# Optimization experiments

Measured on AMD Instinct MI355X. Metric: run time of the kernel, lower is better.

The kernel has to match this reference:

```python
import jax, jax.numpy as jnp
import numpy as np


def setup_inputs() -> dict:
    key = jax.random.key(0)
    kq, kk, kv, km, kb = jax.random.split(key, 5)
    B, H, S, D = 4, 16, 2048, 64
    Q = jax.random.normal(kq, (B, H, S, D), dtype=jnp.float32)
    K = jax.random.normal(kk, (B, H, S, D), dtype=jnp.float32)
    V = jax.random.normal(kv, (B, H, S, D), dtype=jnp.float32)
    # key-padding style mask, broadcasts over query dim; 0 -> masked
    mask = jax.random.randint(km, (B, 1, 1, S), 0, 2, dtype=jnp.int32)
    attn_bias = jax.random.normal(kb, (1, H, S, S), dtype=jnp.float32)
    return {"Q": Q, "K": K, "V": V, "mask": mask, "attn_bias": attn_bias}


def reference(Q, K, V, mask, attn_bias):
    d_k = Q.shape[-1]
    scale = 1.0 / jnp.sqrt(jnp.asarray(d_k, Q.dtype))
    # [B,H,Sq,Sk] scores
    scores = jnp.einsum("bhqd,bhkd->bhqk", Q, K) * scale
    scores = scores + attn_bias
    scores = jnp.where(mask == 0, jnp.asarray(-1e9, scores.dtype), scores)
    attn = jax.nn.softmax(scores, axis=-1)
    # dropout is identity in eval/reference mode
    output = jnp.einsum("bhqk,bhkd->bhqd", attn, V)
    return output, attn
```

## Files before the change

### kernel.cpp

```cpp
#include <hip/hip_runtime.h>

#define NB 4
#define NH 16
#define NS 2048
#define ND 64

typedef __attribute__((ext_vector_type(8))) short short8;
typedef __attribute__((ext_vector_type(4))) short short4v;
typedef __attribute__((ext_vector_type(4))) float floatx4;
typedef __attribute__((ext_vector_type(2))) float floatx2;

__device__ __forceinline__ unsigned short f2bf(float f) {
  unsigned u = __builtin_bit_cast(unsigned, f);
  u = (u + 0x7FFFu + ((u >> 16) & 1u)) >> 16;
  return (unsigned short)u;
}
__device__ __forceinline__ float bf2f(unsigned short s) {
  unsigned u = ((unsigned)s) << 16;
  return __builtin_bit_cast(float, u);
}

__global__ __launch_bounds__(256) void prep_k_kernel(const float* __restrict__ K,
                                                     unsigned short* __restrict__ kb) {
  size_t i = ((size_t)blockIdx.x * 256 + threadIdx.x) * 4;
  floatx4 v = *(const floatx4*)(K + i);
  unsigned long long o = 0;
  o |= (unsigned long long)f2bf(v[0]);
  o |= (unsigned long long)f2bf(v[1]) << 16;
  o |= (unsigned long long)f2bf(v[2]) << 32;
  o |= (unsigned long long)f2bf(v[3]) << 48;
  *(unsigned long long*)(kb + i) = o;
}

__global__ __launch_bounds__(256) void prep_vt_kernel(const float* __restrict__ V,
                                                      unsigned short* __restrict__ vt) {
  __shared__ float tile[64][65];
  int kc = blockIdx.x & 31;
  int bh = blockIdx.x >> 5;
  int k0 = kc * 64;
  const float* src = V + ((size_t)bh * NS + k0) * ND;
  int t = threadIdx.x;
  int r0 = t >> 4;
  int c = (t & 15) * 4;
  for (int rr = 0; rr < 4; ++rr) {
    int r = rr * 16 + r0;
    floatx4 v = *(const floatx4*)(src + (size_t)r * ND + c);
    tile[r][c + 0] = v[0]; tile[r][c + 1] = v[1];
    tile[r][c + 2] = v[2]; tile[r][c + 3] = v[3];
  }
  __syncthreads();
  unsigned short* dst = vt + (size_t)bh * ND * NS + k0;
  for (int i = 0; i < 16; ++i) {
    int lin = i * 256 + t;
    int d = lin >> 6, k = lin & 63;
    dst[(size_t)d * NS + k] = f2bf(tile[k][d]);
  }
}

__global__ __launch_bounds__(1024) void attn_kernel(
    const float* __restrict__ Q,
    const unsigned short* __restrict__ Kb,
    const unsigned short* __restrict__ VT,
    const int* __restrict__ mask,
    const float* __restrict__ bias,
    float* __restrict__ out,
    float* __restrict__ attn) {
  extern __shared__ char smem[];
  unsigned short* P = (unsigned short*)smem;
  float* sums = (float*)(smem + 32 * 2052 * 2);
  const int PST = 2052;

  const int bid = blockIdx.x;
  const int b = bid & 3;
  const int hq = bid >> 2;
  const int qt = hq & 63;
  const int h = hq >> 6;
  const int q0 = qt * 32;

  const int tid = threadIdx.x;
  const int wave = tid >> 6;
  const int lane = tid & 63;
  const int lg = lane >> 4;
  const int lc = lane & 15;
  const int lg4 = lg * 4;
  const int lg8 = lg * 8;

  const size_t bh = (size_t)(b * NH + h);

  short8 aq[2][2];
#pragma unroll
  for (int qh = 0; qh < 2; ++qh) {
    const float* qrow = Q + (bh * NS + (size_t)(q0 + qh * 16 + lc)) * ND + lg8;
#pragma unroll
    for (int t = 0; t < 2; ++t) {
      floatx4 f0 = *(const floatx4*)(qrow + t * 32);
      floatx4 f1 = *(const floatx4*)(qrow + t * 32 + 4);
      short8 a;
      a[0] = (short)f2bf(f0[0]); a[1] = (short)f2bf(f0[1]);
      a[2] = (short)f2bf(f0[2]); a[3] = (short)f2bf(f0[3]);
      a[4] = (short)f2bf(f1[0]); a[5] = (short)f2bf(f1[1]);
      a[6] = (short)f2bf(f1[2]); a[7] = (short)f2bf(f1[3]);
      aq[qh][t] = a;
    }
  }

  const float* bp[2][4];
#pragma unroll
  for (int qh = 0; qh < 2; ++qh)
#pragma unroll
    for (int r = 0; r < 4; ++r)
      bp[qh][r] = bias + ((size_t)h * NS + (size_t)(q0 + qh * 16 + lg4 + r)) * NS + lc;
  const int* mp = mask + b * NS + lc;
  const unsigned short* kp = Kb + bh * NS * ND + (size_t)lc * ND + lg8;

  float psum[2][4] = {{0.f, 0.f, 0.f, 0.f}, {0.f, 0.f, 0.f, 0.f}};
  const int kb0 = wave * 128;

#pragma unroll 2
  for (int it = 0; it < 8; ++it) {
    const int k0 = kb0 + it * 16;
    short8 bk0v = *(const short8*)(kp + (size_t)k0 * ND);
    short8 bk1v = *(const short8*)(kp + (size_t)k0 * ND + 32);
    int mv = mp[k0];
    float bvv[2][4];
#pragma unroll
    for (int qh = 0; qh < 2; ++qh)
#pragma unroll
      for (int r = 0; r < 4; ++r) bvv[qh][r] = bp[qh][r][k0];
#pragma unroll
    for (int qh = 0; qh < 2; ++qh) {
      floatx4 c = {0.f, 0.f, 0.f, 0.f};
      c = __builtin_amdgcn_mfma_f32_16x16x32_bf16(aq[qh][0], bk0v, c, 0, 0, 0);
      c = __builtin_amdgcn_mfma_f32_16x16x32_bf16(aq[qh][1], bk1v, c, 0, 0, 0);
#pragma unroll
      for (int r = 0; r < 4; ++r) {
        float s = c[r] * 0.125f + bvv[qh][r];
        float p = mv ? __expf(s) : 0.f;
        psum[qh][r] += p;
        P[(qh * 16 + lg4 + r) * PST + k0 + lc] = f2bf(p);
      }
    }
  }

#pragma unroll
  for (int qh = 0; qh < 2; ++qh)
#pragma unroll
    for (int r = 0; r < 4; ++r) {
      float v = psum[qh][r];
      v += __shfl_xor(v, 1);
      v += __shfl_xor(v, 2);
      v += __shfl_xor(v, 4);
      v += __shfl_xor(v, 8);
      if (lc == 0) sums[wave * 32 + qh * 16 + lg4 + r] = v;
    }
  __syncthreads();

  {
    const size_t abase = (bh * NS + (size_t)q0) * NS;
#pragma unroll
    for (int rr = 0; rr < 2; ++rr) {
      const int row = wave * 2 + rr;
      float tot = 0.f;
#pragma unroll
      for (int w = 0; w < 16; ++w) tot += sums[w * 32 + row];
      const float inv = 1.f / tot;
      float* arow = attn + abase + (size_t)row * NS;
      const unsigned short* prow = P + row * PST;
#pragma unroll 2
      for (int it = 0; it < 8; ++it) {
        const int col = it * 256 + lane * 4;
        short4v pv = *(const short4v*)(prow + col);
        floatx4 f;
        f[0] = bf2f((unsigned short)pv[0]) * inv;
        f[1] = bf2f((unsigned short)pv[1]) * inv;
        f[2] = bf2f((unsigned short)pv[2]) * inv;
        f[3] = bf2f((unsigned short)pv[3]) * inv;
        *(floatx4*)(arow + col) = f;
      }
    }
  }

  floatx4 o[2][4];
#pragma unroll
  for (int qh = 0; qh < 2; ++qh)
#pragma unroll
    for (int dt = 0; dt < 4; ++dt) o[qh][dt] = (floatx4){0.f, 0.f, 0.f, 0.f};

  const unsigned short* vp = VT + bh * (size_t)ND * NS + (size_t)lc * NS + lg8;
#pragma unroll 2
  for (int it = 0; it < 4; ++it) {
    const int k0 = kb0 + it * 32;
    short8 pa[2];
#pragma unroll
    for (int qh = 0; qh < 2; ++qh) {
      const unsigned short* pr = P + (qh * 16 + lc) * PST + k0 + lg8;
      short4v lo = *(const short4v*)pr;
      short4v hi = *(const short4v*)(pr + 4);
      pa[qh] = __builtin_shufflevector(lo, hi, 0, 1, 2, 3, 4, 5, 6, 7);
    }
#pragma unroll
    for (int dt = 0; dt < 4; ++dt) {
      short8 bb = *(const short8*)(vp + (size_t)(dt * 16) * NS + k0);
#pragma unroll
      for (int qh = 0; qh < 2; ++qh)
        o[qh][dt] = __builtin_amdgcn_mfma_f32_16x16x32_bf16(pa[qh], bb, o[qh][dt], 0, 0, 0);
    }
  }
  __syncthreads();

  float* Ored = (float*)smem;
#pragma unroll
  for (int qh = 0; qh < 2; ++qh)
#pragma unroll
    for (int dt = 0; dt < 4; ++dt)
#pragma unroll
      for (int r = 0; r < 4; ++r)
        Ored[((size_t)wave * 32 + qh * 16 + lg4 + r) * 64 + dt * 16 + lc] = o[qh][dt][r];
  __syncthreads();

  {
    const int q = tid >> 5;
    const int dsub = (tid & 31) * 2;
    floatx2 acc = {0.f, 0.f};
#pragma unroll
    for (int w = 0; w < 16; ++w)
      acc += *(const floatx2*)(Ored + ((size_t)w * 32 + q) * 64 + dsub);
    float tot = 0.f;
#pragma unroll
    for (int w = 0; w < 16; ++w) tot += sums[w * 32 + q];
    const float inv = 1.f / tot;
    floatx2 res;
    res[0] = acc[0] * inv;
    res[1] = acc[1] * inv;
    *(floatx2*)(out + (bh * NS + (size_t)(q0 + q)) * ND + dsub) = res;
  }
}

extern "C" void kernel_launch(void* const* d_in, const int* in_sizes, int n_in,
                              void* d_out, int out_size, void* d_ws, size_t ws_size,
                              hipStream_t stream) {
  const float* Q = (const float*)d_in[0];
  const float* K = (const float*)d_in[1];
  const float* V = (const float*)d_in[2];
  const int* mask = (const int*)d_in[3];
  const float* bias = (const float*)d_in[4];

  float* out = (float*)d_out;
  float* attn = out + (size_t)NB * NH * NS * ND;

  unsigned short* kb = (unsigned short*)d_ws;
  unsigned short* vt = kb + (size_t)NB * NH * NS * ND;

  (void)hipFuncSetAttribute((const void*)attn_kernel,
                            hipFuncAttributeMaxDynamicSharedMemorySize, 133376);

  prep_k_kernel<<<(NB * NH * NS * ND) / (256 * 4), 256, 0, stream>>>(K, kb);
  prep_vt_kernel<<<NB * NH * (NS / 64), 256, 0, stream>>>(V, vt);
  attn_kernel<<<NB * NH * (NS / 32), 1024, 133376, stream>>>(Q, kb, vt, mask, bias, out, attn);
}
```

Baseline: 667.6 us.

## Halve query tile to 16 rows, prefetch K/bias, use nontemporal stores

Each block now handles 16 query rows instead of 32, which halves the LDS footprint (about 66KB) so two 1024-thread blocks can share a CU, and doubles the grid. The QK loop is fully unrolled and software-pipelined: the next K fragments, mask and bias values are loaded while the current MFMAs run. The attn and out writes use nontemporal stores to keep the large attn stream from polluting cache. In exchange, K and V fragments are re-read twice as often across blocks, and each block does less MFMA work per load.

```diff
diff --git a/kernel.cpp b/kernel.cpp
--- a/kernel.cpp
+++ b/kernel.cpp
@@ -4,6 +4,7 @@
 #define NH 16
 #define NS 2048
 #define ND 64
+#define PST 2052
 
 typedef __attribute__((ext_vector_type(8))) short short8;
 typedef __attribute__((ext_vector_type(4))) short short4v;
@@ -57,7 +58,7 @@
   }
 }
 
-__global__ __launch_bounds__(1024) void attn_kernel(
+__global__ __launch_bounds__(1024, 8) void attn_kernel(
     const float* __restrict__ Q,
     const unsigned short* __restrict__ Kb,
     const unsigned short* __restrict__ VT,
@@ -67,15 +68,13 @@
     float* __restrict__ attn) {
   extern __shared__ char smem[];
   unsigned short* P = (unsigned short*)smem;
-  float* sums = (float*)(smem + 32 * 2052 * 2);
-  const int PST = 2052;
+  float* sums = (float*)(smem + 16 * PST * 2);
 
   const int bid = blockIdx.x;
   const int b = bid & 3;
-  const int hq = bid >> 2;
-  const int qt = hq & 63;
-  const int h = hq >> 6;
-  const int q0 = qt * 32;
+  const int qt = (bid >> 2) & 127;
+  const int h = bid >> 9;
+  const int q0 = qt * 16;
 
   const int tid = threadIdx.x;
   const int wave = tid >> 6;
@@ -87,10 +86,9 @@
 
   const size_t bh = (size_t)(b * NH + h);
 
-  short8 aq[2][2];
-#pragma unroll
-  for (int qh = 0; qh < 2; ++qh) {
-    const float* qrow = Q + (bh * NS + (size_t)(q0 + qh * 16 + lc)) * ND + lg8;
+  short8 aq[2];
+  {
+    const float* qrow = Q + (bh * NS + (size_t)(q0 + lc)) * ND + lg8;
 #pragma unroll
     for (int t = 0; t < 2; ++t) {
       floatx4 f0 = *(const floatx4*)(qrow + t * 32);
@@ -100,139 +98,123 @@
       a[2] = (short)f2bf(f0[2]); a[3] = (short)f2bf(f0[3]);
       a[4] = (short)f2bf(f1[0]); a[5] = (short)f2bf(f1[1]);
       a[6] = (short)f2bf(f1[2]); a[7] = (short)f2bf(f1[3]);
-      aq[qh][t] = a;
-    }
-  }
-
-  const float* bp[2][4];
-#pragma unroll
-  for (int qh = 0; qh < 2; ++qh)
-#pragma unroll
-    for (int r = 0; r < 4; ++r)
-      bp[qh][r] = bias + ((size_t)h * NS + (size_t)(q0 + qh * 16 + lg4 + r)) * NS + lc;
+      aq[t] = a;
+    }
+  }
+
+  const unsigned short* kp = Kb + bh * NS * ND + (size_t)lc * ND + lg8;
+  const float* bprow = bias + ((size_t)h * NS + (size_t)(q0 + lg4)) * NS + lc;
   const int* mp = mask + b * NS + lc;
-  const unsigned short* kp = Kb + bh * NS * ND + (size_t)lc * ND + lg8;
-
-  float psum[2][4] = {{0.f, 0.f, 0.f, 0.f}, {0.f, 0.f, 0.f, 0.f}};
+
+  float psum[4] = {0.f, 0.f, 0.f, 0.f};
   const int kb0 = wave * 128;
 
-#pragma unroll 2
+  short8 kfa[2], kfb[2];
+  float bvv[2][4];
+  int mvv[2];
+  {
+    const int k0 = kb0;
+    kfa[0] = *(const short8*)(kp + (size_t)k0 * ND);
+    kfb[0] = *(const short8*)(kp + (size_t)k0 * ND + 32);
+    mvv[0] = mp[k0];
+#pragma unroll
+    for (int r = 0; r < 4; ++r) bvv[0][r] = bprow[(size_t)r * NS + k0];
+  }
+#pragma unroll
   for (int it = 0; it < 8; ++it) {
+    const int cur = it & 1, nxt = cur ^ 1;
+    if (it < 7) {
+      const int k1 = kb0 + (it + 1) * 16;
+      kfa[nxt] = *(const short8*)(kp + (size_t)k1 * ND);
+      kfb[nxt] = *(const short8*)(kp + (size_t)k1 * ND + 32);
+      mvv[nxt] = mp[k1];
+#pragma unroll
+      for (int r = 0; r < 4; ++r) bvv[nxt][r] = bprow[(size_t)r * NS + k1];
+    }
     const int k0 = kb0 + it * 16;
-    short8 bk0v = *(const short8*)(kp + (size_t)k0 * ND);
-    short8 bk1v = *(const short8*)(kp + (size_t)k0 * ND + 32);
-    int mv = mp[k0];
-    float bvv[2][4];
-#pragma unroll
-    for (int qh = 0; qh < 2; ++qh)
-#pragma unroll
-      for (int r = 0; r < 4; ++r) bvv[qh][r] = bp[qh][r][k0];
-#pragma unroll
-    for (int qh = 0; qh < 2; ++qh) {
-      floatx4 c = {0.f, 0.f, 0.f, 0.f};
-      c = __builtin_amdgcn_mfma_f32_16x16x32_bf16(aq[qh][0], bk0v, c, 0, 0, 0);
-      c = __builtin_amdgcn_mfma_f32_16x16x32_bf16(aq[qh][1], bk1v, c, 0, 0, 0);
-#pragma unroll
-      for (int r = 0; r < 4; ++r) {
-        float s = c[r] * 0.125f + bvv[qh][r];
-        float p = mv ? __expf(s) : 0.f;
-        psum[qh][r] += p;
-        P[(qh * 16 + lg4 + r) * PST + k0 + lc] = f2bf(p);
-      }
-    }
-  }
-
-#pragma unroll
-  for (int qh = 0; qh < 2; ++qh)
+    floatx4 c = {0.f, 0.f, 0.f, 0.f};
+    c = __builtin_amdgcn_mfma_f32_16x16x32_bf16(aq[0], kfa[cur], c, 0, 0, 0);
+    c = __builtin_amdgcn_mfma_f32_16x16x32_bf16(aq[1], kfb[cur], c, 0, 0, 0);
 #pragma unroll
     for (int r = 0; r < 4; ++r) {
-      float v = psum[qh][r];
-      v += __shfl_xor(v, 1);
-      v += __shfl_xor(v, 2);
-      v += __shfl_xor(v, 4);
-      v += __shfl_xor(v, 8);
-      if (lc == 0) sums[wave * 32 + qh * 16 + lg4 + r] = v;
-    }
-  __syncthreads();
-
-  {
-    const size_t abase = (bh * NS + (size_t)q0) * NS;
-#pragma unroll
-    for (int rr = 0; rr < 2; ++rr) {
-      const int row = wave * 2 + rr;
-      float tot = 0.f;
-#pragma unroll
-      for (int w = 0; w < 16; ++w) tot += sums[w * 32 + row];
-      const float inv = 1.f / tot;
-      float* arow = attn + abase + (size_t)row * NS;
-      const unsigned short* prow = P + row * PST;
-#pragma unroll 2
-      for (int it = 0; it < 8; ++it) {
-        const int col = it * 256 + lane * 4;
-        short4v pv = *(const short4v*)(prow + col);
-        floatx4 f;
-        f[0] = bf2f((unsigned short)pv[0]) * inv;
-        f[1] = bf2f((unsigned short)pv[1]) * inv;
-        f[2] = bf2f((unsigned short)pv[2]) * inv;
-        f[3] = bf2f((unsigned short)pv[3]) * inv;
-        *(floatx4*)(arow + col) = f;
-      }
-    }
-  }
-
-  floatx4 o[2][4];
-#pragma unroll
-  for (int qh = 0; qh < 2; ++qh)
-#pragma unroll
-    for (int dt = 0; dt < 4; ++dt) o[qh][dt] = (floatx4){0.f, 0.f, 0.f, 0.f};
+      float s = c[r] * 0.125f + bvv[cur][r];
+      float p = mvv[cur] ? __expf(s) : 0.f;
+      psum[r] += p;
+      P[(lg4 + r) * PST + k0 + lc] = f2bf(p);
+    }
+  }
+
+#pragma unroll
+  for (int r = 0; r < 4; ++r) {
+    float v = psum[r];
+    v += __shfl_xor(v, 1);
+    v += __shfl_xor(v, 2);
+    v += __shfl_xor(v, 4);
+    v += __shfl_xor(v, 8);
+    if (lc == 0) sums[wave * 16 + lg4 + r] = v;
+  }
+  __syncthreads();
+
+  {
+    const int row = wave;
+    float tot = 0.f;
+#pragma unroll
+    for (int w = 0; w < 16; ++w) tot += sums[w * 16 + row];
+    const float inv = 1.f / tot;
+    float* arow = attn + (bh * NS + (size_t)(q0 + row)) * NS;
+    const unsigned short* prow = P + row * PST;
+#pragma unroll
+    for (int it = 0; it < 8; ++it) {
+      const int col = it * 256 + lane * 4;
+      short4v pv = *(const short4v*)(prow + col);
+      floatx4 f;
+      f[0] = bf2f((unsigned short)pv[0]) * inv;
+      f[1] = bf2f((unsigned short)pv[1]) * inv;
+      f[2] = bf2f((unsigned short)pv[2]) * inv;
+      f[3] = bf2f((unsigned short)pv[3]) * inv;
+      __builtin_nontemporal_store(f, (floatx4*)(arow + col));
+    }
+  }
+
+  floatx4 o[4];
+#pragma unroll
+  for (int dt = 0; dt < 4; ++dt) o[dt] = (floatx4){0.f, 0.f, 0.f, 0.f};
 
   const unsigned short* vp = VT + bh * (size_t)ND * NS + (size_t)lc * NS + lg8;
-#pragma unroll 2
+#pragma unroll
   for (int it = 0; it < 4; ++it) {
     const int k0 = kb0 + it * 32;
-    short8 pa[2];
-#pragma unroll
-    for (int qh = 0; qh < 2; ++qh) {
-      const unsigned short* pr = P + (qh * 16 + lc) * PST + k0 + lg8;
-      short4v lo = *(const short4v*)pr;
-      short4v hi = *(const short4v*)(pr + 4);
-      pa[qh] = __builtin_shufflevector(lo, hi, 0, 1, 2, 3, 4, 5, 6, 7);
-    }
+    const unsigned short* pr = P + lc * PST + k0 + lg8;
+    short4v lo = *(const short4v*)pr;
+    short4v hi = *(const short4v*)(pr + 4);
+    short8 pa = __builtin_shufflevector(lo, hi, 0, 1, 2, 3, 4, 5, 6, 7);
 #pragma unroll
     for (int dt = 0; dt < 4; ++dt) {
       short8 bb = *(const short8*)(vp + (size_t)(dt * 16) * NS + k0);
-#pragma unroll
-      for (int qh = 0; qh < 2; ++qh)
-        o[qh][dt] = __builtin_amdgcn_mfma_f32_16x16x32_bf16(pa[qh], bb, o[qh][dt], 0, 0, 0);
+      o[dt] = __builtin_amdgcn_mfma_f32_16x16x32_bf16(pa, bb, o[dt], 0, 0, 0);
     }
   }
   __syncthreads();
 
   float* Ored = (float*)smem;
 #pragma unroll
-  for (int qh = 0; qh < 2; ++qh)
-#pragma unroll
-    for (int dt = 0; dt < 4; ++dt)
-#pragma unroll
-      for (int r = 0; r < 4; ++r)
-        Ored[((size_t)wave * 32 + qh * 16 + lg4 + r) * 64 + dt * 16 + lc] = o[qh][dt][r];
-  __syncthreads();
-
-  {
-    const int q = tid >> 5;
-    const int dsub = (tid & 31) * 2;
-    floatx2 acc = {0.f, 0.f};
-#pragma unroll
-    for (int w = 0; w < 16; ++w)
-      acc += *(const floatx2*)(Ored + ((size_t)w * 32 + q) * 64 + dsub);
+  for (int dt = 0; dt < 4; ++dt)
+#pragma unroll
+    for (int r = 0; r < 4; ++r)
+      Ored[((size_t)wave * 16 + lg4 + r) * 64 + dt * 16 + lc] = o[dt][r];
+  __syncthreads();
+
+  {
+    const int q = tid >> 6;
+    const int col = tid & 63;
+    float acc = 0.f;
+#pragma unroll
+    for (int w = 0; w < 16; ++w) acc += Ored[((size_t)w * 16 + q) * 64 + col];
     float tot = 0.f;
 #pragma unroll
-    for (int w = 0; w < 16; ++w) tot += sums[w * 32 + q];
+    for (int w = 0; w < 16; ++w) tot += sums[w * 16 + q];
     const float inv = 1.f / tot;
-    floatx2 res;
-    res[0] = acc[0] * inv;
-    res[1] = acc[1] * inv;
-    *(floatx2*)(out + (bh * NS + (size_t)(q0 + q)) * ND + dsub) = res;
+    __builtin_nontemporal_store(acc * inv, out + (bh * NS + (size_t)(q0 + q)) * ND + col);
   }
 }
 
@@ -251,10 +233,11 @@
   unsigned short* kb = (unsigned short*)d_ws;
   unsigned short* vt = kb + (size_t)NB * NH * NS * ND;
 
+  const int lds_bytes = 16 * PST * 2 + 16 * 16 * 4;
   (void)hipFuncSetAttribute((const void*)attn_kernel,
-                            hipFuncAttributeMaxDynamicSharedMemorySize, 133376);
+                            hipFuncAttributeMaxDynamicSharedMemorySize, lds_bytes);
 
   prep_k_kernel<<<(NB * NH * NS * ND) / (256 * 4), 256, 0, stream>>>(K, kb);
   prep_vt_kernel<<<NB * NH * (NS / 64), 256, 0, stream>>>(V, vt);
-  attn_kernel<<<NB * NH * (NS / 32), 1024, 133376, stream>>>(Q, kb, vt, mask, bias, out, attn);
-}
+  attn_kernel<<<NB * NH * (NS / 16), 1024, lds_bytes, stream>>>(Q, kb, vt, mask, bias, out, attn);
+}
```

Result: slower. 738.8 us (+10.7%).
